# Performance work log

Hardware: AMD Instinct MI355X
Metric: run time of the kernel (lower is better)

## Reference

```python
import jax, jax.numpy as jnp
import numpy as np

B, S, D, H = 8, 2048, 768, 12

def setup_inputs() -> dict:
    key = jax.random.key(0)
    kx, km, kk, kq, kv = jax.random.split(key, 5)
    return {
        "x": jax.random.normal(kx, (B, S, D), dtype=jnp.float32),
        "mask": jax.random.randint(km, (B, 1, S), 0, 2, dtype=jnp.int32),
        "key_weight": jax.random.normal(kk, (D, H), dtype=jnp.float32),
        "query_weight": jax.random.normal(kq, (D, H), dtype=jnp.float32),
        "value_weight": jax.random.normal(kv, (D, H), dtype=jnp.float32),
    }

def reference(x, mask, key_weight, query_weight, value_weight):
    scale = 1.0 / (key_weight.shape[-1] ** 0.5)
    k = jnp.einsum('bsd,dh->bsh', x, key_weight)
    q = jnp.einsum('bsd,dh->bsh', x, query_weight)
    v = jnp.einsum('bsd,dh->bsh', x, value_weight)
    # scores: (B, S, T) — full score matrix as in the original
    scores = jnp.einsum('bsh,bth->bst', q, k) * scale
    scores = jnp.where(mask == 0, -jnp.inf, scores)
    attn = jax.nn.softmax(scores, axis=-1)
    return jnp.einsum('bst,bth->bsh', attn, v)
```

## Files before the change

### kernel.cpp

```cpp
#include <hip/hip_runtime.h>
#include <math.h>

#define QSCALE (0.2886751345948129f * 1.4426950408889634f)

#if __has_builtin(__builtin_amdgcn_exp2f)
#define EXP2F(x) __builtin_amdgcn_exp2f(x)
#else
#define EXP2F(x) exp2f(x)
#endif

typedef __attribute__((ext_vector_type(8))) _Float16 half8;
typedef __attribute__((ext_vector_type(4))) _Float16 half4_t;
typedef __attribute__((ext_vector_type(4))) float floatx4;

#define MFMA32F16(a, b, c) __builtin_amdgcn_mfma_f32_16x16x32_f16((a), (b), (c), 0, 0, 0)
#define MFMA16F16(a, b, c) __builtin_amdgcn_mfma_f32_16x16x16f16((a), (b), (c), 0, 0, 0)

static __device__ inline float bperm(float v, int addr_bytes) {
    return __int_as_float(__builtin_amdgcn_ds_bpermute(addr_bytes, __float_as_int(v)));
}

__global__ __launch_bounds__(256)
void prep(const float* __restrict__ Wq, const float* __restrict__ Wk,
          const float* __restrict__ Wv, const int* __restrict__ mask,
          _Float16* __restrict__ wfh, _Float16* __restrict__ wfl,
          int* __restrict__ dst, int* __restrict__ nvalid,
          float4* __restrict__ zbase)
{
    const int b = blockIdx.x;
    const int tid = threadIdx.x;
    if (b < 18) {
        int t = b * 256 + tid;
        if (t >= 4608) return;
        int lane = t & 63;
        int nt   = (t >> 6) % 3;
        int ks   = t / 192;
        const float* W = (nt == 0) ? Wq : (nt == 1) ? Wk : Wv;
        const float scale = (nt == 0) ? QSCALE : 1.0f;
        int col = lane & 15;
        int q8  = lane >> 4;
        half8 hi, lo;
        #pragma unroll
        for (int j = 0; j < 8; ++j) {
            int dim = ks * 32 + q8 * 8 + j;
            float f = (col < 12) ? W[dim * 12 + col] * scale : 0.0f;
            _Float16 h = (_Float16)f;
            hi[j] = h;
            lo[j] = (_Float16)(f - (float)h);
        }
        size_t off = ((size_t)(ks * 3 + nt) * 64 + lane) * 8;
        *(half8*)(wfh + off) = hi;
        *(half8*)(wfl + off) = lo;
    } else if (b < 26) {
        __shared__ int cnt[256];
        const int bb = b - 18;
        const int* mb = mask + bb * 2048;
        int local[8]; int c = 0;
        #pragma unroll
        for (int i = 0; i < 8; ++i) { local[i] = (mb[tid * 8 + i] != 0); c += local[i]; }
        cnt[tid] = c;
        __syncthreads();
        for (int off = 1; off < 256; off <<= 1) {
            int u = cnt[tid];
            int add = (tid >= off) ? cnt[tid - off] : 0;
            __syncthreads();
            cnt[tid] = u + add;
            __syncthreads();
        }
        int run = (tid == 0) ? 0 : cnt[tid - 1];
        int* db = dst + bb * 2048;
        #pragma unroll
        for (int i = 0; i < 8; ++i) { db[tid * 8 + i] = local[i] ? run : -1; run += local[i]; }
        if (tid == 255) nvalid[bb] = cnt[255];
    } else {
        const float4 z = make_float4(0.f, 0.f, 0.f, 0.f);
        for (int i = (b - 26) * 256 + tid; i < 163840; i += 6 * 256) zbase[i] = z;
    }
}

__global__ __launch_bounds__(256, 3)
void qkv_mfma(const float* __restrict__ x, const _Float16* __restrict__ wfh,
              const _Float16* __restrict__ wfl, const int* __restrict__ dst,
              _Float16* __restrict__ qfh, _Float16* __restrict__ qfl,
              _Float16* __restrict__ kfh, _Float16* __restrict__ kfl,
              _Float16* __restrict__ vtf)
{
    __shared__ __align__(16) float cbuf[3072];
    const int tid  = threadIdx.x;
    const int lane = tid & 63;
    const int w    = tid >> 6;
    const int g    = blockIdx.x;
    const int rowbase = g * 16;
    const int m15 = lane & 15;
    const int q8  = lane >> 4;

    const float* xbase = x + (size_t)(rowbase + m15) * 768 + q8 * 8;
    const half8* WH = (const half8*)wfh;
    const half8* WL = (const half8*)wfl;

    float xv[6][8];
    #pragma unroll
    for (int s = 0; s < 6; ++s) {
        const int ks = w * 6 + s;
        *(float4*)(xv[s])     = *(const float4*)(xbase + ks * 32);
        *(float4*)(xv[s] + 4) = *(const float4*)(xbase + ks * 32 + 4);
    }

    floatx4 acc0 = {0.f, 0.f, 0.f, 0.f};
    floatx4 acc1 = acc0, acc2 = acc0;

    half8 bh[2][3], bl[2][3];
    {
        const int ks = w * 6;
        #pragma unroll
        for (int n = 0; n < 3; ++n) {
            bh[0][n] = WH[(ks * 3 + n) * 64 + lane];
            bl[0][n] = WL[(ks * 3 + n) * 64 + lane];
        }
    }

    #pragma unroll
    for (int s = 0; s < 6; ++s) {
        const int cur = s & 1, nxt = cur ^ 1;
        if (s < 5) {
            const int ksn = w * 6 + s + 1;
            #pragma unroll
            for (int n = 0; n < 3; ++n) {
                bh[nxt][n] = WH[(ksn * 3 + n) * 64 + lane];
                bl[nxt][n] = WL[(ksn * 3 + n) * 64 + lane];
            }
        }
        half8 ah, al;
        #pragma unroll
        for (int j = 0; j < 8; ++j) {
            _Float16 h = (_Float16)xv[s][j];
            ah[j] = h;
            al[j] = (_Float16)(xv[s][j] - (float)h);
        }
        acc0 = MFMA32F16(ah, bh[cur][0], acc0);
        acc1 = MFMA32F16(ah, bh[cur][1], acc1);
        acc2 = MFMA32F16(ah, bh[cur][2], acc2);
        acc0 = MFMA32F16(al, bh[cur][0], acc0);
        acc1 = MFMA32F16(al, bh[cur][1], acc1);
        acc2 = MFMA32F16(al, bh[cur][2], acc2);
        acc0 = MFMA32F16(ah, bl[cur][0], acc0);
        acc1 = MFMA32F16(ah, bl[cur][1], acc1);
        acc2 = MFMA32F16(ah, bl[cur][2], acc2);
    }

    *(floatx4*)(cbuf + ((w * 3 + 0) * 64 + lane) * 4) = acc0;
    *(floatx4*)(cbuf + ((w * 3 + 1) * 64 + lane) * 4) = acc1;
    *(floatx4*)(cbuf + ((w * 3 + 2) * 64 + lane) * 4) = acc2;
    __syncthreads();
    if (w < 3) {
        floatx4 t0 = *(const floatx4*)(cbuf + ((0 * 3 + w) * 64 + lane) * 4);
        floatx4 t1 = *(const floatx4*)(cbuf + ((1 * 3 + w) * 64 + lane) * 4);
        floatx4 t2 = *(const floatx4*)(cbuf + ((2 * 3 + w) * 64 + lane) * 4);
        floatx4 t3 = *(const floatx4*)(cbuf + ((3 * 3 + w) * 64 + lane) * 4);
        floatx4 tot = t0 + t1 + t2 + t3;
        const int col = m15;
        const int r0  = q8 * 4;
        #pragma unroll
        for (int r = 0; r < 4; ++r) {
            const int row = rowbase + r0 + r;
            const float val = tot[r];
            if (w == 0) {
                if (col < 12) {
                    size_t off = ((size_t)g * 64 + (col >> 3) * 16 + (r0 + r)) * 8 + (col & 7);
                    _Float16 h = (_Float16)val;
                    qfh[off] = h;
                    qfl[off] = (_Float16)(val - (float)h);
                }
            } else {
                const int d = dst[row];
                if (d >= 0) {
                    const int bb = row >> 11;
                    if (w == 1) {
                        if (col < 12) {
                            size_t off = (((size_t)(bb * 128 + (d >> 4))) * 64
                                          + (col >> 3) * 16 + (d & 15)) * 8 + (col & 7);
                            _Float16 h = (_Float16)val;
                            kfh[off] = h;
                            kfl[off] = (_Float16)(val - (float)h);
                        }
                    } else {
                        if (col < 12) {
                            size_t off = (((size_t)(bb * 128 + (d >> 4))) * 64
                                          + ((d & 15) >> 2) * 16 + col) * 4 + (d & 3);
                            vtf[off] = (_Float16)val;
                        } else if (col == 12) {
                            size_t off = (((size_t)(bb * 128 + (d >> 4))) * 64
                                          + ((d & 15) >> 2) * 16 + 12) * 4 + (d & 3);
                            vtf[off] = (_Float16)1.0f;
                        }
                    }
                }
            }
        }
    }
}

__global__ __launch_bounds__(256)
void attn(const _Float16* __restrict__ qfh, const _Float16* __restrict__ qfl,
          const _Float16* __restrict__ kfh, const _Float16* __restrict__ kfl,
          const _Float16* __restrict__ vtf, const int* __restrict__ nvalid,
          float* __restrict__ out)
{
    __shared__ float cm[512];
    __shared__ __align__(16) floatx4 co[512];
    const int tid  = threadIdx.x;
    const int lane = tid & 63;
    const int w    = tid >> 6;
    const int bb   = blockIdx.x & 7;
    const int gl   = blockIdx.x >> 3;
    const int g0   = bb * 128 + gl * 2;
    const int m15  = lane & 15;

    const half8 qh0 = *(const half8*)(qfh + ((size_t)g0 * 64 + lane) * 8);
    const half8 ql0 = *(const half8*)(qfl + ((size_t)g0 * 64 + lane) * 8);
    const half8 qh1 = *(const half8*)(qfh + ((size_t)(g0 + 1) * 64 + lane) * 8);
    const half8 ql1 = *(const half8*)(qfl + ((size_t)(g0 + 1) * 64 + lane) * 8);

    const half8* KH = (const half8*)kfh + (size_t)bb * 128 * 64;
    const half8* KL = (const half8*)kfl + (size_t)bb * 128 * 64;
    const half4_t* VT = (const half4_t*)vtf + (size_t)bb * 128 * 64;

    const int nv = nvalid[bb];
    const int nt = (nv + 15) >> 4;
    const int a16 = (lane ^ 16) << 2;
    const int a32 = (lane ^ 32) << 2;

    float m0 = -INFINITY, m1 = -INFINITY;
    floatx4 o0 = {0.f, 0.f, 0.f, 0.f};
    floatx4 o1 = o0;

    int t = w;
    half8 kh, kl;
    half4_t va;
    if (t < nt) {
        kh = KH[t * 64 + lane];
        kl = KL[t * 64 + lane];
        va = VT[t * 64 + lane];
    }
    for (; t < nt; t += 4) {
        half8 nkh, nkl; half4_t nva;
        if (t + 4 < nt) {
            nkh = KH[(t + 4) * 64 + lane];
            nkl = KL[(t + 4) * 64 + lane];
            nva = VT[(t + 4) * 64 + lane];
        }
        floatx4 s0 = {0.f, 0.f, 0.f, 0.f};
        floatx4 s1 = s0;
        s0 = MFMA32F16(kh, qh0, s0);
        s1 = MFMA32F16(kh, qh1, s1);
        s0 = MFMA32F16(kl, qh0, s0);
        s1 = MFMA32F16(kl, qh1, s1);
        s0 = MFMA32F16(kh, ql0, s0);
        s1 = MFMA32F16(kh, ql1, s1);
        {
            float pm = fmaxf(fmaxf(s0.x, s0.y), fmaxf(s0.z, s0.w));
            pm = fmaxf(pm, bperm(pm, a16));
            pm = fmaxf(pm, bperm(pm, a32));
            float mnew = fmaxf(m0, pm);
            float corr = EXP2F(m0 - mnew);
            o0.x *= corr; o0.y *= corr; o0.z *= corr; o0.w *= corr;
            half4_t pb;
            pb[0] = (_Float16)EXP2F(s0.x - mnew);
            pb[1] = (_Float16)EXP2F(s0.y - mnew);
            pb[2] = (_Float16)EXP2F(s0.z - mnew);
            pb[3] = (_Float16)EXP2F(s0.w - mnew);
            o0 = MFMA16F16(va, pb, o0);
            m0 = mnew;
        }
        {
            float pm = fmaxf(fmaxf(s1.x, s1.y), fmaxf(s1.z, s1.w));
            pm = fmaxf(pm, bperm(pm, a16));
            pm = fmaxf(pm, bperm(pm, a32));
            float mnew = fmaxf(m1, pm);
            float corr = EXP2F(m1 - mnew);
            o1.x *= corr; o1.y *= corr; o1.z *= corr; o1.w *= corr;
            half4_t pb;
            pb[0] = (_Float16)EXP2F(s1.x - mnew);
            pb[1] = (_Float16)EXP2F(s1.y - mnew);
            pb[2] = (_Float16)EXP2F(s1.z - mnew);
            pb[3] = (_Float16)EXP2F(s1.w - mnew);
            o1 = MFMA16F16(va, pb, o1);
            m1 = mnew;
        }
        kh = nkh; kl = nkl; va = nva;
    }

    cm[(0 * 4 + w) * 64 + lane] = m0;
    cm[(1 * 4 + w) * 64 + lane] = m1;
    co[(0 * 4 + w) * 64 + lane] = o0;
    co[(1 * 4 + w) * 64 + lane] = o1;
    __syncthreads();
    if (w < 2) {
        const int gi = w;
        float gm = -INFINITY;
        #pragma unroll
        for (int w2 = 0; w2 < 4; ++w2) gm = fmaxf(gm, cm[(gi * 4 + w2) * 64 + lane]);
        floatx4 O = {0.f, 0.f, 0.f, 0.f};
        #pragma unroll
        for (int w2 = 0; w2 < 4; ++w2) {
            float f = EXP2F(cm[(gi * 4 + w2) * 64 + lane] - gm);
            floatx4 ow = co[(gi * 4 + w2) * 64 + lane];
            O.x += ow.x * f; O.y += ow.y * f; O.z += ow.z * f; O.w += ow.w * f;
        }
        float L = bperm(O.x, (48 + m15) << 2);
        float inv = 1.0f / L;
        if ((lane >> 4) < 3) {
            float4 ov = make_float4(O.x * inv, O.y * inv, O.z * inv, O.w * inv);
            *(float4*)(out + ((size_t)(g0 + gi) * 16 + m15) * 12 + (lane >> 4) * 4) = ov;
        }
    }
}

extern "C" void kernel_launch(void* const* d_in, const int* in_sizes, int n_in,
                              void* d_out, int out_size, void* d_ws, size_t ws_size,
                              hipStream_t stream) {
    const float* x    = (const float*)d_in[0];
    const int*   mask = (const int*)  d_in[1];
    const float* Wk   = (const float*)d_in[2];
    const float* Wq   = (const float*)d_in[3];
    const float* Wv   = (const float*)d_in[4];
    float* out = (float*)d_out;

    char* base = (char*)d_ws;
    _Float16* qfh = (_Float16*)(base);
    _Float16* qfl = (_Float16*)(base + (1u << 20));
    _Float16* kfh = (_Float16*)(base + (2u << 20));
    _Float16* kfl = (_Float16*)(base + (3u << 20));
    _Float16* vtf = (_Float16*)(base + (4u << 20));
    _Float16* wfh = (_Float16*)(base + 4718592);
    _Float16* wfl = (_Float16*)(base + 4718592 + 73728);
    int* dst      = (int*)(base + 4866048);
    int* nvalid   = (int*)(base + 4866048 + 65536);
    float4* zbase = (float4*)(base + (2u << 20));

    prep<<<32, 256, 0, stream>>>(Wq, Wk, Wv, mask, wfh, wfl, dst, nvalid, zbase);
    qkv_mfma<<<1024, 256, 0, stream>>>(x, wfh, wfl, dst, qfh, qfl, kfh, kfl, vtf);
    attn<<<512, 256, 0, stream>>>(qfh, qfl, kfh, kfl, vtf, nvalid, out);
}
```

Baseline: 113.3 us.

## Fuse prep, QKV projection and attention into one cooperative kernel with grid syncs

Merges the three kernels into a single cooperative launch of 512 blocks that uses grid.sync between the prep, projection and attention phases. Each block now projects two 16-row groups, since the grid shrank from 1024 to 512 blocks. The aim is to remove two kernel-launch gaps and the tail effects between dependent kernels. In exchange it adds grid-wide barrier costs, raises register pressure, and limits occupancy because the whole grid must stay resident.

```diff
diff --git a/kernel.cpp b/kernel.cpp
--- a/kernel.cpp
+++ b/kernel.cpp
@@ -1,5 +1,8 @@
 #include <hip/hip_runtime.h>
+#include <hip/hip_cooperative_groups.h>
 #include <math.h>
+
+namespace cg = cooperative_groups;
 
 #define QSCALE (0.2886751345948129f * 1.4426950408889634f)
 
@@ -20,40 +23,52 @@
     return __int_as_float(__builtin_amdgcn_ds_bpermute(addr_bytes, __float_as_int(v)));
 }
 
-__global__ __launch_bounds__(256)
-void prep(const float* __restrict__ Wq, const float* __restrict__ Wk,
-          const float* __restrict__ Wv, const int* __restrict__ mask,
-          _Float16* __restrict__ wfh, _Float16* __restrict__ wfl,
-          int* __restrict__ dst, int* __restrict__ nvalid,
-          float4* __restrict__ zbase)
+__global__ __launch_bounds__(256, 2)
+void fused(const float* __restrict__ x, const int* __restrict__ mask,
+           const float* __restrict__ Wq, const float* __restrict__ Wk,
+           const float* __restrict__ Wv,
+           _Float16* __restrict__ wfh, _Float16* __restrict__ wfl,
+           int* __restrict__ dst, int* __restrict__ nvalid,
+           _Float16* __restrict__ qfh, _Float16* __restrict__ qfl,
+           _Float16* __restrict__ kfh, _Float16* __restrict__ kfl,
+           _Float16* __restrict__ vtf, float4* __restrict__ zbase,
+           float* __restrict__ out)
 {
-    const int b = blockIdx.x;
-    const int tid = threadIdx.x;
-    if (b < 18) {
-        int t = b * 256 + tid;
-        if (t >= 4608) return;
-        int lane = t & 63;
-        int nt   = (t >> 6) % 3;
-        int ks   = t / 192;
-        const float* W = (nt == 0) ? Wq : (nt == 1) ? Wk : Wv;
-        const float scale = (nt == 0) ? QSCALE : 1.0f;
-        int col = lane & 15;
-        int q8  = lane >> 4;
-        half8 hi, lo;
-        #pragma unroll
-        for (int j = 0; j < 8; ++j) {
-            int dim = ks * 32 + q8 * 8 + j;
-            float f = (col < 12) ? W[dim * 12 + col] * scale : 0.0f;
-            _Float16 h = (_Float16)f;
-            hi[j] = h;
-            lo[j] = (_Float16)(f - (float)h);
-        }
-        size_t off = ((size_t)(ks * 3 + nt) * 64 + lane) * 8;
-        *(half8*)(wfh + off) = hi;
-        *(half8*)(wfl + off) = lo;
-    } else if (b < 26) {
-        __shared__ int cnt[256];
-        const int bb = b - 18;
+    __shared__ __align__(16) float smem[6144];
+    cg::grid_group grid = cg::this_grid();
+    const int blk  = blockIdx.x;
+    const int tid  = threadIdx.x;
+    const int lane = tid & 63;
+    const int w    = tid >> 6;
+    const int m15  = lane & 15;
+    const int q8   = lane >> 4;
+
+    if (blk < 18) {
+        int t = blk * 256 + tid;
+        if (t < 4608) {
+            int l2 = t & 63;
+            int nt = (t >> 6) % 3;
+            int ks = t / 192;
+            const float* W = (nt == 0) ? Wq : (nt == 1) ? Wk : Wv;
+            const float scale = (nt == 0) ? QSCALE : 1.0f;
+            int col = l2 & 15;
+            int kq  = l2 >> 4;
+            half8 hi, lo;
+            #pragma unroll
+            for (int j = 0; j < 8; ++j) {
+                int dim = ks * 32 + kq * 8 + j;
+                float f = (col < 12) ? W[dim * 12 + col] * scale : 0.0f;
+                _Float16 h = (_Float16)f;
+                hi[j] = h;
+                lo[j] = (_Float16)(f - (float)h);
+            }
+            size_t off = ((size_t)(ks * 3 + nt) * 64 + l2) * 8;
+            *(half8*)(wfh + off) = hi;
+            *(half8*)(wfl + off) = lo;
+        }
+    } else if (blk < 26) {
+        int* cnt = (int*)smem;
+        const int bb = blk - 18;
         const int* mb = mask + bb * 2048;
         int local[8]; int c = 0;
         #pragma unroll
@@ -72,246 +87,250 @@
         #pragma unroll
         for (int i = 0; i < 8; ++i) { db[tid * 8 + i] = local[i] ? run : -1; run += local[i]; }
         if (tid == 255) nvalid[bb] = cnt[255];
-    } else {
+    } else if (blk >= 32) {
         const float4 z = make_float4(0.f, 0.f, 0.f, 0.f);
-        for (int i = (b - 26) * 256 + tid; i < 163840; i += 6 * 256) zbase[i] = z;
+        for (int i = (blk - 32) * 256 + tid; i < 163840; i += 480 * 256) zbase[i] = z;
     }
-}
-
-__global__ __launch_bounds__(256, 3)
-void qkv_mfma(const float* __restrict__ x, const _Float16* __restrict__ wfh,
-              const _Float16* __restrict__ wfl, const int* __restrict__ dst,
-              _Float16* __restrict__ qfh, _Float16* __restrict__ qfl,
-              _Float16* __restrict__ kfh, _Float16* __restrict__ kfl,
-              _Float16* __restrict__ vtf)
-{
-    __shared__ __align__(16) float cbuf[3072];
-    const int tid  = threadIdx.x;
-    const int lane = tid & 63;
-    const int w    = tid >> 6;
-    const int g    = blockIdx.x;
-    const int rowbase = g * 16;
-    const int m15 = lane & 15;
-    const int q8  = lane >> 4;
-
-    const float* xbase = x + (size_t)(rowbase + m15) * 768 + q8 * 8;
-    const half8* WH = (const half8*)wfh;
-    const half8* WL = (const half8*)wfl;
-
-    float xv[6][8];
-    #pragma unroll
-    for (int s = 0; s < 6; ++s) {
-        const int ks = w * 6 + s;
-        *(float4*)(xv[s])     = *(const float4*)(xbase + ks * 32);
-        *(float4*)(xv[s] + 4) = *(const float4*)(xbase + ks * 32 + 4);
-    }
-
-    floatx4 acc0 = {0.f, 0.f, 0.f, 0.f};
-    floatx4 acc1 = acc0, acc2 = acc0;
-
-    half8 bh[2][3], bl[2][3];
+    __threadfence();
+    grid.sync();
+
     {
-        const int ks = w * 6;
-        #pragma unroll
-        for (int n = 0; n < 3; ++n) {
-            bh[0][n] = WH[(ks * 3 + n) * 64 + lane];
-            bl[0][n] = WL[(ks * 3 + n) * 64 + lane];
-        }
-    }
-
-    #pragma unroll
-    for (int s = 0; s < 6; ++s) {
-        const int cur = s & 1, nxt = cur ^ 1;
-        if (s < 5) {
-            const int ksn = w * 6 + s + 1;
+        const int g0 = blk * 2;
+        const float* xb0 = x + (size_t)(g0 * 16 + m15) * 768 + q8 * 8;
+        const float* xb1 = xb0 + 16 * 768;
+        const half8* WH = (const half8*)wfh;
+        const half8* WL = (const half8*)wfl;
+
+        float xv0[6][8], xv1[6][8];
+        #pragma unroll
+        for (int s = 0; s < 6; ++s) {
+            const int ks = w * 6 + s;
+            *(float4*)(xv0[s])     = *(const float4*)(xb0 + ks * 32);
+            *(float4*)(xv0[s] + 4) = *(const float4*)(xb0 + ks * 32 + 4);
+            *(float4*)(xv1[s])     = *(const float4*)(xb1 + ks * 32);
+            *(float4*)(xv1[s] + 4) = *(const float4*)(xb1 + ks * 32 + 4);
+        }
+
+        floatx4 acc[2][3];
+        #pragma unroll
+        for (int gi = 0; gi < 2; ++gi)
+            #pragma unroll
+            for (int n = 0; n < 3; ++n) acc[gi][n] = (floatx4){0.f, 0.f, 0.f, 0.f};
+
+        half8 bh[2][3], bl[2][3];
+        {
+            const int ks = w * 6;
             #pragma unroll
             for (int n = 0; n < 3; ++n) {
-                bh[nxt][n] = WH[(ksn * 3 + n) * 64 + lane];
-                bl[nxt][n] = WL[(ksn * 3 + n) * 64 + lane];
-            }
-        }
-        half8 ah, al;
-        #pragma unroll
-        for (int j = 0; j < 8; ++j) {
-            _Float16 h = (_Float16)xv[s][j];
-            ah[j] = h;
-            al[j] = (_Float16)(xv[s][j] - (float)h);
-        }
-        acc0 = MFMA32F16(ah, bh[cur][0], acc0);
-        acc1 = MFMA32F16(ah, bh[cur][1], acc1);
-        acc2 = MFMA32F16(ah, bh[cur][2], acc2);
-        acc0 = MFMA32F16(al, bh[cur][0], acc0);
-        acc1 = MFMA32F16(al, bh[cur][1], acc1);
-        acc2 = MFMA32F16(al, bh[cur][2], acc2);
-        acc0 = MFMA32F16(ah, bl[cur][0], acc0);
-        acc1 = MFMA32F16(ah, bl[cur][1], acc1);
-        acc2 = MFMA32F16(ah, bl[cur][2], acc2);
-    }
-
-    *(floatx4*)(cbuf + ((w * 3 + 0) * 64 + lane) * 4) = acc0;
-    *(floatx4*)(cbuf + ((w * 3 + 1) * 64 + lane) * 4) = acc1;
-    *(floatx4*)(cbuf + ((w * 3 + 2) * 64 + lane) * 4) = acc2;
-    __syncthreads();
-    if (w < 3) {
-        floatx4 t0 = *(const floatx4*)(cbuf + ((0 * 3 + w) * 64 + lane) * 4);
-        floatx4 t1 = *(const floatx4*)(cbuf + ((1 * 3 + w) * 64 + lane) * 4);
-        floatx4 t2 = *(const floatx4*)(cbuf + ((2 * 3 + w) * 64 + lane) * 4);
-        floatx4 t3 = *(const floatx4*)(cbuf + ((3 * 3 + w) * 64 + lane) * 4);
-        floatx4 tot = t0 + t1 + t2 + t3;
-        const int col = m15;
-        const int r0  = q8 * 4;
-        #pragma unroll
-        for (int r = 0; r < 4; ++r) {
-            const int row = rowbase + r0 + r;
-            const float val = tot[r];
-            if (w == 0) {
-                if (col < 12) {
-                    size_t off = ((size_t)g * 64 + (col >> 3) * 16 + (r0 + r)) * 8 + (col & 7);
-                    _Float16 h = (_Float16)val;
-                    qfh[off] = h;
-                    qfl[off] = (_Float16)(val - (float)h);
+                bh[0][n] = WH[(ks * 3 + n) * 64 + lane];
+                bl[0][n] = WL[(ks * 3 + n) * 64 + lane];
+            }
+        }
+
+        #pragma unroll
+        for (int s = 0; s < 6; ++s) {
+            const int cur = s & 1, nxt = cur ^ 1;
+            if (s < 5) {
+                const int ksn = w * 6 + s + 1;
+                #pragma unroll
+                for (int n = 0; n < 3; ++n) {
+                    bh[nxt][n] = WH[(ksn * 3 + n) * 64 + lane];
+                    bl[nxt][n] = WL[(ksn * 3 + n) * 64 + lane];
                 }
-            } else {
-                const int d = dst[row];
-                if (d >= 0) {
-                    const int bb = row >> 11;
-                    if (w == 1) {
+            }
+            half8 ah0, al0, ah1, al1;
+            #pragma unroll
+            for (int j = 0; j < 8; ++j) {
+                _Float16 h0 = (_Float16)xv0[s][j];
+                ah0[j] = h0;
+                al0[j] = (_Float16)(xv0[s][j] - (float)h0);
+                _Float16 h1 = (_Float16)xv1[s][j];
+                ah1[j] = h1;
+                al1[j] = (_Float16)(xv1[s][j] - (float)h1);
+            }
+            #pragma unroll
+            for (int n = 0; n < 3; ++n) {
+                acc[0][n] = MFMA32F16(ah0, bh[cur][n], acc[0][n]);
+                acc[1][n] = MFMA32F16(ah1, bh[cur][n], acc[1][n]);
+            }
+            #pragma unroll
+            for (int n = 0; n < 3; ++n) {
+                acc[0][n] = MFMA32F16(al0, bh[cur][n], acc[0][n]);
+                acc[1][n] = MFMA32F16(al1, bh[cur][n], acc[1][n]);
+            }
+            #pragma unroll
+            for (int n = 0; n < 3; ++n) {
+                acc[0][n] = MFMA32F16(ah0, bl[cur][n], acc[0][n]);
+                acc[1][n] = MFMA32F16(ah1, bl[cur][n], acc[1][n]);
+            }
+        }
+
+        #pragma unroll
+        for (int gi = 0; gi < 2; ++gi)
+            #pragma unroll
+            for (int n = 0; n < 3; ++n)
+                *(floatx4*)(smem + (((gi * 4 + w) * 3 + n) * 64 + lane) * 4) = acc[gi][n];
+        __syncthreads();
+        if (w < 3) {
+            #pragma unroll
+            for (int gi = 0; gi < 2; ++gi) {
+                floatx4 tot = (floatx4){0.f, 0.f, 0.f, 0.f};
+                #pragma unroll
+                for (int w2 = 0; w2 < 4; ++w2) {
+                    floatx4 t = *(const floatx4*)(smem + (((gi * 4 + w2) * 3 + w) * 64 + lane) * 4);
+                    tot.x += t.x; tot.y += t.y; tot.z += t.z; tot.w += t.w;
+                }
+                const int g   = g0 + gi;
+                const int col = m15;
+                const int r0  = q8 * 4;
+                #pragma unroll
+                for (int r = 0; r < 4; ++r) {
+                    const int row = g * 16 + r0 + r;
+                    const float val = tot[r];
+                    if (w == 0) {
                         if (col < 12) {
-                            size_t off = (((size_t)(bb * 128 + (d >> 4))) * 64
-                                          + (col >> 3) * 16 + (d & 15)) * 8 + (col & 7);
+                            size_t off = ((size_t)g * 64 + (col >> 3) * 16 + (r0 + r)) * 8 + (col & 7);
                             _Float16 h = (_Float16)val;
-                            kfh[off] = h;
-                            kfl[off] = (_Float16)(val - (float)h);
+                            qfh[off] = h;
+                            qfl[off] = (_Float16)(val - (float)h);
                         }
                     } else {
-                        if (col < 12) {
-                            size_t off = (((size_t)(bb * 128 + (d >> 4))) * 64
-                                          + ((d & 15) >> 2) * 16 + col) * 4 + (d & 3);
-                            vtf[off] = (_Float16)val;
-                        } else if (col == 12) {
-                            size_t off = (((size_t)(bb * 128 + (d >> 4))) * 64
-                                          + ((d & 15) >> 2) * 16 + 12) * 4 + (d & 3);
-                            vtf[off] = (_Float16)1.0f;
+                        const int d = dst[row];
+                        if (d >= 0) {
+                            const int bb = row >> 11;
+                            if (w == 1) {
+                                if (col < 12) {
+                                    size_t off = (((size_t)(bb * 128 + (d >> 4))) * 64
+                                                  + (col >> 3) * 16 + (d & 15)) * 8 + (col & 7);
+                                    _Float16 h = (_Float16)val;
+                                    kfh[off] = h;
+                                    kfl[off] = (_Float16)(val - (float)h);
+                                }
+                            } else {
+                                if (col < 12) {
+                                    size_t off = (((size_t)(bb * 128 + (d >> 4))) * 64
+                                                  + ((d & 15) >> 2) * 16 + col) * 4 + (d & 3);
+                                    vtf[off] = (_Float16)val;
+                                } else if (col == 12) {
+                                    size_t off = (((size_t)(bb * 128 + (d >> 4))) * 64
+                                                  + ((d & 15) >> 2) * 16 + 12) * 4 + (d & 3);
+                                    vtf[off] = (_Float16)1.0f;
+                                }
+                            }
                         }
                     }
                 }
             }
         }
     }
-}
-
-__global__ __launch_bounds__(256)
-void attn(const _Float16* __restrict__ qfh, const _Float16* __restrict__ qfl,
-          const _Float16* __restrict__ kfh, const _Float16* __restrict__ kfl,
-          const _Float16* __restrict__ vtf, const int* __restrict__ nvalid,
-          float* __restrict__ out)
-{
-    __shared__ float cm[512];
-    __shared__ __align__(16) floatx4 co[512];
-    const int tid  = threadIdx.x;
-    const int lane = tid & 63;
-    const int w    = tid >> 6;
-    const int bb   = blockIdx.x & 7;
-    const int gl   = blockIdx.x >> 3;
-    const int g0   = bb * 128 + gl * 2;
-    const int m15  = lane & 15;
-
-    const half8 qh0 = *(const half8*)(qfh + ((size_t)g0 * 64 + lane) * 8);
-    const half8 ql0 = *(const half8*)(qfl + ((size_t)g0 * 64 + lane) * 8);
-    const half8 qh1 = *(const half8*)(qfh + ((size_t)(g0 + 1) * 64 + lane) * 8);
-    const half8 ql1 = *(const half8*)(qfl + ((size_t)(g0 + 1) * 64 + lane) * 8);
-
-    const half8* KH = (const half8*)kfh + (size_t)bb * 128 * 64;
-    const half8* KL = (const half8*)kfl + (size_t)bb * 128 * 64;
-    const half4_t* VT = (const half4_t*)vtf + (size_t)bb * 128 * 64;
-
-    const int nv = nvalid[bb];
-    const int nt = (nv + 15) >> 4;
-    const int a16 = (lane ^ 16) << 2;
-    const int a32 = (lane ^ 32) << 2;
-
-    float m0 = -INFINITY, m1 = -INFINITY;
-    floatx4 o0 = {0.f, 0.f, 0.f, 0.f};
-    floatx4 o1 = o0;
-
-    int t = w;
-    half8 kh, kl;
-    half4_t va;
-    if (t < nt) {
-        kh = KH[t * 64 + lane];
-        kl = KL[t * 64 + lane];
-        va = VT[t * 64 + lane];
-    }
-    for (; t < nt; t += 4) {
-        half8 nkh, nkl; half4_t nva;
-        if (t + 4 < nt) {
-            nkh = KH[(t + 4) * 64 + lane];
-            nkl = KL[(t + 4) * 64 + lane];
-            nva = VT[(t + 4) * 64 + lane];
-        }
-        floatx4 s0 = {0.f, 0.f, 0.f, 0.f};
-        floatx4 s1 = s0;
-        s0 = MFMA32F16(kh, qh0, s0);
-        s1 = MFMA32F16(kh, qh1, s1);
-        s0 = MFMA32F16(kl, qh0, s0);
-        s1 = MFMA32F16(kl, qh1, s1);
-        s0 = MFMA32F16(kh, ql0, s0);
-        s1 = MFMA32F16(kh, ql1, s1);
-        {
-            float pm = fmaxf(fmaxf(s0.x, s0.y), fmaxf(s0.z, s0.w));
-            pm = fmaxf(pm, bperm(pm, a16));
-            pm = fmaxf(pm, bperm(pm, a32));
-            float mnew = fmaxf(m0, pm);
-            float corr = EXP2F(m0 - mnew);
-            o0.x *= corr; o0.y *= corr; o0.z *= corr; o0.w *= corr;
-            half4_t pb;
-            pb[0] = (_Float16)EXP2F(s0.x - mnew);
-            pb[1] = (_Float16)EXP2F(s0.y - mnew);
-            pb[2] = (_Float16)EXP2F(s0.z - mnew);
-            pb[3] = (_Float16)EXP2F(s0.w - mnew);
-            o0 = MFMA16F16(va, pb, o0);
-            m0 = mnew;
-        }
-        {
-            float pm = fmaxf(fmaxf(s1.x, s1.y), fmaxf(s1.z, s1.w));
-            pm = fmaxf(pm, bperm(pm, a16));
-            pm = fmaxf(pm, bperm(pm, a32));
-            float mnew = fmaxf(m1, pm);
-            float corr = EXP2F(m1 - mnew);
-            o1.x *= corr; o1.y *= corr; o1.z *= corr; o1.w *= corr;
-            half4_t pb;
-            pb[0] = (_Float16)EXP2F(s1.x - mnew);
-            pb[1] = (_Float16)EXP2F(s1.y - mnew);
-            pb[2] = (_Float16)EXP2F(s1.z - mnew);
-            pb[3] = (_Float16)EXP2F(s1.w - mnew);
-            o1 = MFMA16F16(va, pb, o1);
-            m1 = mnew;
-        }
-        kh = nkh; kl = nkl; va = nva;
-    }
-
-    cm[(0 * 4 + w) * 64 + lane] = m0;
-    cm[(1 * 4 + w) * 64 + lane] = m1;
-    co[(0 * 4 + w) * 64 + lane] = o0;
-    co[(1 * 4 + w) * 64 + lane] = o1;
-    __syncthreads();
-    if (w < 2) {
-        const int gi = w;
-        float gm = -INFINITY;
-        #pragma unroll
-        for (int w2 = 0; w2 < 4; ++w2) gm = fmaxf(gm, cm[(gi * 4 + w2) * 64 + lane]);
-        floatx4 O = {0.f, 0.f, 0.f, 0.f};
-        #pragma unroll
-        for (int w2 = 0; w2 < 4; ++w2) {
-            float f = EXP2F(cm[(gi * 4 + w2) * 64 + lane] - gm);
-            floatx4 ow = co[(gi * 4 + w2) * 64 + lane];
-            O.x += ow.x * f; O.y += ow.y * f; O.z += ow.z * f; O.w += ow.w * f;
-        }
-        float L = bperm(O.x, (48 + m15) << 2);
-        float inv = 1.0f / L;
-        if ((lane >> 4) < 3) {
-            float4 ov = make_float4(O.x * inv, O.y * inv, O.z * inv, O.w * inv);
-            *(float4*)(out + ((size_t)(g0 + gi) * 16 + m15) * 12 + (lane >> 4) * 4) = ov;
+    __threadfence();
+    grid.sync();
+
+    {
+        float* cm = smem;
+        floatx4* co = (floatx4*)(smem + 512);
+        const int bb = blk & 7;
+        const int gl = blk >> 3;
+        const int g0 = bb * 128 + gl * 2;
+
+        const half8 qh0 = *(const half8*)(qfh + ((size_t)g0 * 64 + lane) * 8);
+        const half8 ql0 = *(const half8*)(qfl + ((size_t)g0 * 64 + lane) * 8);
+        const half8 qh1 = *(const half8*)(qfh + ((size_t)(g0 + 1) * 64 + lane) * 8);
+        const half8 ql1 = *(const half8*)(qfl + ((size_t)(g0 + 1) * 64 + lane) * 8);
+
+        const half8* KH = (const half8*)kfh + (size_t)bb * 128 * 64;
+        const half8* KL = (const half8*)kfl + (size_t)bb * 128 * 64;
+        const half4_t* VT = (const half4_t*)vtf + (size_t)bb * 128 * 64;
+
+        const int nv = nvalid[bb];
+        const int nt = (nv + 15) >> 4;
+        const int a16 = (lane ^ 16) << 2;
+        const int a32 = (lane ^ 32) << 2;
+
+        float m0 = -INFINITY, m1 = -INFINITY;
+        floatx4 o0 = {0.f, 0.f, 0.f, 0.f};
+        floatx4 o1 = o0;
+
+        int t = w;
+        half8 kh, kl;
+        half4_t va;
+        if (t < nt) {
+            kh = KH[t * 64 + lane];
+            kl = KL[t * 64 + lane];
+            va = VT[t * 64 + lane];
+        }
+        for (; t < nt; t += 4) {
+            half8 nkh, nkl; half4_t nva;
+            if (t + 4 < nt) {
+                nkh = KH[(t + 4) * 64 + lane];
+                nkl = KL[(t + 4) * 64 + lane];
+                nva = VT[(t + 4) * 64 + lane];
+            }
+            floatx4 s0 = {0.f, 0.f, 0.f, 0.f};
+            floatx4 s1 = s0;
+            s0 = MFMA32F16(kh, qh0, s0);
+            s1 = MFMA32F16(kh, qh1, s1);
+            s0 = MFMA32F16(kl, qh0, s0);
+            s1 = MFMA32F16(kl, qh1, s1);
+            s0 = MFMA32F16(kh, ql0, s0);
+            s1 = MFMA32F16(kh, ql1, s1);
+            {
+                float pm = fmaxf(fmaxf(s0.x, s0.y), fmaxf(s0.z, s0.w));
+                pm = fmaxf(pm, bperm(pm, a16));
+                pm = fmaxf(pm, bperm(pm, a32));
+                float mnew = fmaxf(m0, pm);
+                float corr = EXP2F(m0 - mnew);
+                o0.x *= corr; o0.y *= corr; o0.z *= corr; o0.w *= corr;
+                half4_t pb;
+                pb[0] = (_Float16)EXP2F(s0.x - mnew);
+                pb[1] = (_Float16)EXP2F(s0.y - mnew);
+                pb[2] = (_Float16)EXP2F(s0.z - mnew);
+                pb[3] = (_Float16)EXP2F(s0.w - mnew);
+                o0 = MFMA16F16(va, pb, o0);
+                m0 = mnew;
+            }
+            {
+                float pm = fmaxf(fmaxf(s1.x, s1.y), fmaxf(s1.z, s1.w));
+                pm = fmaxf(pm, bperm(pm, a16));
+                pm = fmaxf(pm, bperm(pm, a32));
+                float mnew = fmaxf(m1, pm);
+                float corr = EXP2F(m1 - mnew);
+                o1.x *= corr; o1.y *= corr; o1.z *= corr; o1.w *= corr;
+                half4_t pb;
+                pb[0] = (_Float16)EXP2F(s1.x - mnew);
+                pb[1] = (_Float16)EXP2F(s1.y - mnew);
+                pb[2] = (_Float16)EXP2F(s1.z - mnew);
+                pb[3] = (_Float16)EXP2F(s1.w - mnew);
+                o1 = MFMA16F16(va, pb, o1);
+                m1 = mnew;
+            }
+            kh = nkh; kl = nkl; va = nva;
+        }
+
+        __syncthreads();
+        cm[(0 * 4 + w) * 64 + lane] = m0;
+        cm[(1 * 4 + w) * 64 + lane] = m1;
+        co[(0 * 4 + w) * 64 + lane] = o0;
+        co[(1 * 4 + w) * 64 + lane] = o1;
+        __syncthreads();
+        if (w < 2) {
+            const int gi = w;
+            float gm = -INFINITY;
+            #pragma unroll
+            for (int w2 = 0; w2 < 4; ++w2) gm = fmaxf(gm, cm[(gi * 4 + w2) * 64 + lane]);
+            floatx4 O = {0.f, 0.f, 0.f, 0.f};
+            #pragma unroll
+            for (int w2 = 0; w2 < 4; ++w2) {
+                float f = EXP2F(cm[(gi * 4 + w2) * 64 + lane] - gm);
+                floatx4 ow = co[(gi * 4 + w2) * 64 + lane];
+                O.x += ow.x * f; O.y += ow.y * f; O.z += ow.z * f; O.w += ow.w * f;
+            }
+            float L = bperm(O.x, (48 + m15) << 2);
+            float inv = 1.0f / L;
+            if ((lane >> 4) < 3) {
+                float4 ov = make_float4(O.x * inv, O.y * inv, O.z * inv, O.w * inv);
+                *(float4*)(out + ((size_t)(g0 + gi) * 16 + m15) * 12 + (lane >> 4) * 4) = ov;
+            }
         }
     }
 }
@@ -338,7 +357,11 @@
     int* nvalid   = (int*)(base + 4866048 + 65536);
     float4* zbase = (float4*)(base + (2u << 20));
 
-    prep<<<32, 256, 0, stream>>>(Wq, Wk, Wv, mask, wfh, wfl, dst, nvalid, zbase);
-    qkv_mfma<<<1024, 256, 0, stream>>>(x, wfh, wfl, dst, qfh, qfl, kfh, kfl, vtf);
-    attn<<<512, 256, 0, stream>>>(qfh, qfl, kfh, kfl, vtf, nvalid, out);
+    void* args[16] = {
+        (void*)&x, (void*)&mask, (void*)&Wq, (void*)&Wk, (void*)&Wv,
+        (void*)&wfh, (void*)&wfl, (void*)&dst, (void*)&nvalid,
+        (void*)&qfh, (void*)&qfl, (void*)&kfh, (void*)&kfl, (void*)&vtf,
+        (void*)&zbase, (void*)&out
+    };
+    hipLaunchCooperativeKernel((const void*)fused, dim3(512), dim3(256), args, 0, stream);
 }
```

Measured after the change: 327.0 us. +188.6%, slower.

## Replace mask compaction with in-place zeroed masked keys and full tile loop

Applied to the files above, without the earlier changes.

Removes the prefix-scan compaction of valid keys and the workspace zeroing from the prep kernel. Masked keys and values are instead written as zeros in place, with the softmax denominator column zeroed. Attention now iterates over all 128 key tiles per batch instead of only the valid ones. This simplifies prep and removes the dst lookup, but roughly doubles the attention work for a half-valid mask.

```diff
diff --git a/kernel.cpp b/kernel.cpp
--- a/kernel.cpp
+++ b/kernel.cpp
@@ -22,65 +22,35 @@
 
 __global__ __launch_bounds__(256)
 void prep(const float* __restrict__ Wq, const float* __restrict__ Wk,
-          const float* __restrict__ Wv, const int* __restrict__ mask,
-          _Float16* __restrict__ wfh, _Float16* __restrict__ wfl,
-          int* __restrict__ dst, int* __restrict__ nvalid,
-          float4* __restrict__ zbase)
+          const float* __restrict__ Wv, _Float16* __restrict__ wfh,
+          _Float16* __restrict__ wfl)
 {
-    const int b = blockIdx.x;
-    const int tid = threadIdx.x;
-    if (b < 18) {
-        int t = b * 256 + tid;
-        if (t >= 4608) return;
-        int lane = t & 63;
-        int nt   = (t >> 6) % 3;
-        int ks   = t / 192;
-        const float* W = (nt == 0) ? Wq : (nt == 1) ? Wk : Wv;
-        const float scale = (nt == 0) ? QSCALE : 1.0f;
-        int col = lane & 15;
-        int q8  = lane >> 4;
-        half8 hi, lo;
-        #pragma unroll
-        for (int j = 0; j < 8; ++j) {
-            int dim = ks * 32 + q8 * 8 + j;
-            float f = (col < 12) ? W[dim * 12 + col] * scale : 0.0f;
-            _Float16 h = (_Float16)f;
-            hi[j] = h;
-            lo[j] = (_Float16)(f - (float)h);
-        }
-        size_t off = ((size_t)(ks * 3 + nt) * 64 + lane) * 8;
-        *(half8*)(wfh + off) = hi;
-        *(half8*)(wfl + off) = lo;
-    } else if (b < 26) {
-        __shared__ int cnt[256];
-        const int bb = b - 18;
-        const int* mb = mask + bb * 2048;
-        int local[8]; int c = 0;
-        #pragma unroll
-        for (int i = 0; i < 8; ++i) { local[i] = (mb[tid * 8 + i] != 0); c += local[i]; }
-        cnt[tid] = c;
-        __syncthreads();
-        for (int off = 1; off < 256; off <<= 1) {
-            int u = cnt[tid];
-            int add = (tid >= off) ? cnt[tid - off] : 0;
-            __syncthreads();
-            cnt[tid] = u + add;
-            __syncthreads();
-        }
-        int run = (tid == 0) ? 0 : cnt[tid - 1];
-        int* db = dst + bb * 2048;
-        #pragma unroll
-        for (int i = 0; i < 8; ++i) { db[tid * 8 + i] = local[i] ? run : -1; run += local[i]; }
-        if (tid == 255) nvalid[bb] = cnt[255];
-    } else {
-        const float4 z = make_float4(0.f, 0.f, 0.f, 0.f);
-        for (int i = (b - 26) * 256 + tid; i < 163840; i += 6 * 256) zbase[i] = z;
-    }
+    int t = blockIdx.x * 256 + threadIdx.x;
+    if (t >= 4608) return;
+    int lane = t & 63;
+    int nt   = (t >> 6) % 3;
+    int ks   = t / 192;
+    const float* W = (nt == 0) ? Wq : (nt == 1) ? Wk : Wv;
+    const float scale = (nt == 0) ? QSCALE : 1.0f;
+    int col = lane & 15;
+    int kq  = lane >> 4;
+    half8 hi, lo;
+    #pragma unroll
+    for (int j = 0; j < 8; ++j) {
+        int dim = ks * 32 + kq * 8 + j;
+        float f = (col < 12) ? W[dim * 12 + col] * scale : 0.0f;
+        _Float16 h = (_Float16)f;
+        hi[j] = h;
+        lo[j] = (_Float16)(f - (float)h);
+    }
+    size_t off = ((size_t)(ks * 3 + nt) * 64 + lane) * 8;
+    *(half8*)(wfh + off) = hi;
+    *(half8*)(wfl + off) = lo;
 }
 
 __global__ __launch_bounds__(256, 3)
 void qkv_mfma(const float* __restrict__ x, const _Float16* __restrict__ wfh,
-              const _Float16* __restrict__ wfl, const int* __restrict__ dst,
+              const _Float16* __restrict__ wfl, const int* __restrict__ mask,
               _Float16* __restrict__ qfh, _Float16* __restrict__ qfl,
               _Float16* __restrict__ kfh, _Float16* __restrict__ kfl,
               _Float16* __restrict__ vtf)
@@ -172,28 +142,27 @@
                     qfl[off] = (_Float16)(val - (float)h);
                 }
             } else {
-                const int d = dst[row];
-                if (d >= 0) {
-                    const int bb = row >> 11;
-                    if (w == 1) {
-                        if (col < 12) {
-                            size_t off = (((size_t)(bb * 128 + (d >> 4))) * 64
-                                          + (col >> 3) * 16 + (d & 15)) * 8 + (col & 7);
-                            _Float16 h = (_Float16)val;
-                            kfh[off] = h;
-                            kfl[off] = (_Float16)(val - (float)h);
-                        }
-                    } else {
-                        if (col < 12) {
-                            size_t off = (((size_t)(bb * 128 + (d >> 4))) * 64
-                                          + ((d & 15) >> 2) * 16 + col) * 4 + (d & 3);
-                            vtf[off] = (_Float16)val;
-                        } else if (col == 12) {
-                            size_t off = (((size_t)(bb * 128 + (d >> 4))) * 64
-                                          + ((d & 15) >> 2) * 16 + 12) * 4 + (d & 3);
-                            vtf[off] = (_Float16)1.0f;
-                        }
-                    }
+                const int d   = row & 2047;
+                const int bb  = row >> 11;
+                const int msk = mask[row];
+                const size_t tb = ((size_t)(bb * 128 + (d >> 4))) * 64;
+                if (w == 1) {
+                    float vv = (msk && col < 12) ? val : 0.f;
+                    _Float16 h  = (_Float16)vv;
+                    _Float16 lo = (_Float16)(vv - (float)h);
+                    size_t off1 = (tb + (col >> 3) * 16 + (d & 15)) * 8 + (col & 7);
+                    size_t off2 = (tb + ((col >> 3) + 2) * 16 + (d & 15)) * 8 + (col & 7);
+                    kfh[off1] = h;
+                    kfl[off1] = lo;
+                    kfh[off2] = (_Float16)0.f;
+                    kfl[off2] = (_Float16)0.f;
+                } else {
+                    float vv;
+                    if (col < 12)       vv = msk ? val : 0.f;
+                    else if (col == 12) vv = msk ? 1.f : 0.f;
+                    else                vv = 0.f;
+                    size_t off = (tb + ((d & 15) >> 2) * 16 + col) * 4 + (d & 3);
+                    vtf[off] = (_Float16)vv;
                 }
             }
         }
@@ -203,8 +172,7 @@
 __global__ __launch_bounds__(256)
 void attn(const _Float16* __restrict__ qfh, const _Float16* __restrict__ qfl,
           const _Float16* __restrict__ kfh, const _Float16* __restrict__ kfl,
-          const _Float16* __restrict__ vtf, const int* __restrict__ nvalid,
-          float* __restrict__ out)
+          const _Float16* __restrict__ vtf, float* __restrict__ out)
 {
     __shared__ float cm[512];
     __shared__ __align__(16) floatx4 co[512];
@@ -225,8 +193,6 @@
     const half8* KL = (const half8*)kfl + (size_t)bb * 128 * 64;
     const half4_t* VT = (const half4_t*)vtf + (size_t)bb * 128 * 64;
 
-    const int nv = nvalid[bb];
-    const int nt = (nv + 15) >> 4;
     const int a16 = (lane ^ 16) << 2;
     const int a32 = (lane ^ 32) << 2;
 
@@ -235,16 +201,12 @@
     floatx4 o1 = o0;
 
     int t = w;
-    half8 kh, kl;
-    half4_t va;
-    if (t < nt) {
-        kh = KH[t * 64 + lane];
-        kl = KL[t * 64 + lane];
-        va = VT[t * 64 + lane];
-    }
-    for (; t < nt; t += 4) {
+    half8 kh = KH[t * 64 + lane];
+    half8 kl = KL[t * 64 + lane];
+    half4_t va = VT[t * 64 + lane];
+    for (; t < 128; t += 4) {
         half8 nkh, nkl; half4_t nva;
-        if (t + 4 < nt) {
+        if (t + 4 < 128) {
             nkh = KH[(t + 4) * 64 + lane];
             nkl = KL[(t + 4) * 64 + lane];
             nva = VT[(t + 4) * 64 + lane];
@@ -334,11 +296,8 @@
     _Float16* vtf = (_Float16*)(base + (4u << 20));
     _Float16* wfh = (_Float16*)(base + 4718592);
     _Float16* wfl = (_Float16*)(base + 4718592 + 73728);
-    int* dst      = (int*)(base + 4866048);
-    int* nvalid   = (int*)(base + 4866048 + 65536);
-    float4* zbase = (float4*)(base + (2u << 20));
-
-    prep<<<32, 256, 0, stream>>>(Wq, Wk, Wv, mask, wfh, wfl, dst, nvalid, zbase);
-    qkv_mfma<<<1024, 256, 0, stream>>>(x, wfh, wfl, dst, qfh, qfl, kfh, kfl, vtf);
-    attn<<<512, 256, 0, stream>>>(qfh, qfl, kfh, kfl, vtf, nvalid, out);
-}
+
+    prep<<<18, 256, 0, stream>>>(Wq, Wk, Wv, wfh, wfl);
+    qkv_mfma<<<1024, 256, 0, stream>>>(x, wfh, wfl, mask, qfh, qfl, kfh, kfl, vtf);
+    attn<<<512, 256, 0, stream>>>(qfh, qfl, kfh, kfl, vtf, out);
+}
```

Measured after the change: 124.2 us. +9.6%, slower.
